# Kernel optimization log

Measured on AMD Instinct MI355X. Metric: run time of the kernel, lower is better.

Reference implementation:

```python
import jax, jax.numpy as jnp
import numpy as np

N = 100_000      # nodes
E = 20_000       # hyperedges
NNZ = 1_600_000  # pins (node, hyperedge) pairs
D_IN, D_HID, D_OUT = 128, 128, 64
EPS = 1e-5
NEG_SLOPE = 0.01


def _glorot(key, shape):
    fan_in, fan_out = shape
    lim = np.sqrt(6.0 / (fan_in + fan_out)).astype(np.float32)
    return jax.random.uniform(key, shape, jnp.float32, -lim, lim)


def setup_inputs() -> dict:
    key = jax.random.key(0)
    k = jax.random.split(key, 5)
    x = jax.random.normal(k[0], (N, D_IN), jnp.float32)
    node_idx = jax.random.randint(k[1], (NNZ,), 0, N)
    edge_idx = jax.random.randint(k[2], (NNZ,), 0, E)
    hyperedge_index = jnp.stack([node_idx, edge_idx]).astype(jnp.int64)
    return {
        "x": x,
        "hyperedge_index": hyperedge_index,
        "W1": _glorot(k[3], (D_IN, D_HID)),
        "b1": jnp.zeros((D_HID,), jnp.float32),
        "gamma": jnp.ones((D_HID,), jnp.float32),
        "beta": jnp.zeros((D_HID,), jnp.float32),
        "W3": _glorot(k[4], (D_HID, D_OUT)),
        "b3": jnp.zeros((D_OUT,), jnp.float32),
    }


def hypergraph_conv(x, node_idx, edge_idx, W, b):
    """PyG HypergraphConv (no attention, unit hyperedge weights):
    out = D^-1 H B H^T (x W) + b."""
    x = x @ W  # [N, F]
    ones = jnp.ones(node_idx.shape[0], x.dtype)
    Bdeg = jax.ops.segment_sum(ones, edge_idx, num_segments=E)  # hyperedge degree
    Ddeg = jax.ops.segment_sum(ones, node_idx, num_segments=N)  # node degree
    Binv = jnp.where(Bdeg > 0, 1.0 / Bdeg, 0.0)
    Dinv = jnp.where(Ddeg > 0, 1.0 / Ddeg, 0.0)
    # node -> hyperedge aggregation, scaled by B
    m = jax.ops.segment_sum(x[node_idx], edge_idx, num_segments=E) * Binv[:, None]
    # hyperedge -> node aggregation, scaled by D
    out = jax.ops.segment_sum(m[edge_idx], node_idx, num_segments=N) * Dinv[:, None]
    return out + b


def layer_norm(h, gamma, beta):
    mu = jnp.mean(h, axis=-1, keepdims=True)
    var = jnp.mean(jnp.square(h - mu), axis=-1, keepdims=True)
    return (h - mu) * jax.lax.rsqrt(var + EPS) * gamma + beta


def reference(x, hyperedge_index, W1, b1, gamma, beta, W3, b3):
    node_idx = hyperedge_index[0]
    edge_idx = hyperedge_index[1]
    h = hypergraph_conv(x, node_idx, edge_idx, W1, b1)
    h = layer_norm(h, gamma, beta)
    h = jax.nn.leaky_relu(h, NEG_SLOPE)
    # dropout is identity in eval mode
    z = hypergraph_conv(h, node_idx, edge_idx, W3, b3)
    return z
```

## Files before the change

### kernel.cpp

```cpp
#include <hip/hip_runtime.h>
#include <hip/hip_bf16.h>

#define NNODES 100000
#define NEDGES 20000
#define NPINS  1600000

#define EB_SHIFT 6
#define NB_SHIFT 7
#define NB_E ((NEDGES + 63) / 64)
#define NB_N ((NNODES + 127) / 128)
#define NB_TOT (NB_E + NB_N)
#define ECAP 6144
#define NCAP 2560
#define REG_TOTAL (NB_E * ECAP + NB_N * NCAP)

typedef __attribute__((ext_vector_type(8))) short short8;
typedef __attribute__((ext_vector_type(4))) float f32x4;
typedef unsigned int uint;


static __device__ inline float bf_lo(uint u) { return __uint_as_float(u << 16); }
static __device__ inline float bf_hi(uint u) { return __uint_as_float(u & 0xffff0000u); }

static __device__ inline uint pack_bf2(float a, float b) {
    union { __hip_bfloat16 h; unsigned short u; } ua, ub;
    ua.h = __float2bfloat16(a);
    ub.h = __float2bfloat16(b);
    return ((uint)ub.u << 16) | (uint)ua.u;
}


__global__ void __launch_bounds__(1024) bin_scatter(const int* __restrict__ he,
                                                    int* __restrict__ ccnt,
                                                    uint* __restrict__ pairs) {
    __shared__ int hcnt[NB_TOT];
    __shared__ int hbase[NB_TOT];
    int tid = threadIdx.x;
    int base = blockIdx.x * 8192;
    for (int j = tid; j < NB_TOT; j += 1024) hcnt[j] = 0;
    __syncthreads();
#pragma unroll
    for (int k = 0; k < 8; k++) {
        int i = base + k * 1024 + tid;
        if (i < NPINS) {
            int n = he[i];
            int e = he[NPINS + i];
            atomicAdd(&hcnt[e >> EB_SHIFT], 1);
            atomicAdd(&hcnt[NB_E + (n >> NB_SHIFT)], 1);
        }
    }
    __syncthreads();
    for (int j = tid; j < NB_TOT; j += 1024)
        hbase[j] = hcnt[j] ? atomicAdd(&ccnt[j], hcnt[j]) : 0;
    __syncthreads();
#pragma unroll
    for (int k = 0; k < 8; k++) {
        int i = base + k * 1024 + tid;
        if (i < NPINS) {
            int n = he[i];
            int e = he[NPINS + i];
            int be = e >> EB_SHIFT;
            int pe = atomicAdd(&hbase[be], 1);
            if (pe < ECAP)
                pairs[be * ECAP + pe] = ((uint)(e & 63) << 20) | (uint)n;
            int bn = n >> NB_SHIFT;
            int pn = atomicAdd(&hbase[NB_E + bn], 1);
            if (pn < NCAP)
                pairs[NB_E * ECAP + bn * NCAP + pn] = ((uint)(n & 127) << 20) | (uint)e;
        }
    }
}


template <int COLS, bool BF16IN>
static __device__ __forceinline__ void gemm_body(const void* __restrict__ Xv,
                                                 const float* __restrict__ W,
                                                 unsigned short* __restrict__ Yb,
                                                 long rowbase, char* lds) {
    char* Xl = lds;
    char* Wt = lds + 128 * 256;
    int tid = threadIdx.x;

    if constexpr (!BF16IN) {
        const float4* X4 = reinterpret_cast<const float4*>(Xv);
#pragma unroll
        for (int i = 0; i < 16; i++) {
            int f = tid + i * 256;
            int r = f >> 5;
            int c4 = f & 31;
            long gr = rowbase + r;
            if (gr > NNODES - 1) gr = NNODES - 1;
            float4 v = X4[gr * 32 + c4];
            uint lo = pack_bf2(v.x, v.y);
            uint hi = pack_bf2(v.z, v.w);
            int byte = r * 256 + ((c4 * 8) ^ ((r & 7) << 4));
            *reinterpret_cast<uint2*>(Xl + byte) = make_uint2(lo, hi);
        }
    } else {
        const uint4* X4 = reinterpret_cast<const uint4*>(Xv);
#pragma unroll
        for (int i = 0; i < 8; i++) {
            int f = tid + i * 256;
            int r = f >> 4;
            int c = f & 15;
            long gr = rowbase + r;
            if (gr > NNODES - 1) gr = NNODES - 1;
            uint4 v = X4[gr * 16 + c];
            int byte = r * 256 + ((c * 16) ^ ((r & 7) << 4));
            *reinterpret_cast<uint4*>(Xl + byte) = v;
        }
    }
    for (int f = tid; f < 128 * COLS / 4; f += 256) {
        int k = f / (COLS / 4);
        int c4 = f % (COLS / 4);
        float4 v = reinterpret_cast<const float4*>(W)[f];
        float vv[4] = {v.x, v.y, v.z, v.w};
#pragma unroll
        for (int j = 0; j < 4; j++) {
            int c = c4 * 4 + j;
            union { __hip_bfloat16 h; short s; } u;
            u.h = __float2bfloat16(vv[j]);
            int byte = c * 256 + ((k * 2) ^ ((c & 7) << 4));
            *reinterpret_cast<short*>(Wt + byte) = u.s;
        }
    }
    __syncthreads();

    constexpr int NF = COLS / 16;
    int wave = tid >> 6;
    int lane = tid & 63;
    int lrow = lane & 15;
    int lq = lane >> 4;
    f32x4 acc[2][NF] = {};

#pragma unroll
    for (int ks = 0; ks < 4; ks++) {
        short8 a[2];
#pragma unroll
        for (int rt = 0; rt < 2; rt++) {
            int r = wave * 32 + rt * 16 + lrow;
            int byte = r * 256 + ((ks * 64 + lq * 16) ^ ((r & 7) << 4));
            a[rt] = *reinterpret_cast<const short8*>(Xl + byte);
        }
#pragma unroll
        for (int nf = 0; nf < NF; nf++) {
            int c = nf * 16 + lrow;
            int byte = c * 256 + ((ks * 64 + lq * 16) ^ ((c & 7) << 4));
            short8 b = *reinterpret_cast<const short8*>(Wt + byte);
            acc[0][nf] = __builtin_amdgcn_mfma_f32_16x16x32_bf16(a[0], b, acc[0][nf], 0, 0, 0);
            acc[1][nf] = __builtin_amdgcn_mfma_f32_16x16x32_bf16(a[1], b, acc[1][nf], 0, 0, 0);
        }
    }

#pragma unroll
    for (int rt = 0; rt < 2; rt++)
#pragma unroll
        for (int nf = 0; nf < NF; nf++)
#pragma unroll
            for (int r = 0; r < 4; r++) {
                long row = rowbase + wave * 32 + rt * 16 + lq * 4 + r;
                if (row < NNODES) {
                    union { __hip_bfloat16 h; unsigned short u; } u;
                    u.h = __float2bfloat16(acc[rt][nf][r]);
                    Yb[row * COLS + nf * 16 + lrow] = u.u;
                }
            }
}

__global__ void gemm1_kernel(const float* __restrict__ x, const float* __restrict__ W,
                             unsigned short* __restrict__ Yb) {
    __shared__ __align__(16) char lds[128 * 256 + 128 * 256];
    gemm_body<128, false>(x, W, Yb, (long)blockIdx.x * 128, lds);
}

__global__ void gemm2_kernel(const void* __restrict__ Xv, const float* __restrict__ W,
                             unsigned short* __restrict__ Yb) {
    __shared__ __align__(16) char lds[128 * 256 + 64 * 256];
    gemm_body<64, true>(Xv, W, Yb, (long)blockIdx.x * 128, lds);
}


template <int KPB, int CAP>
static __device__ __forceinline__ void place_body(const uint* __restrict__ pairs, int regbase,
                                                  const int* __restrict__ ccnt, int cbase,
                                                  int kfine_base, int nkeys,
                                                  int* __restrict__ off, int* __restrict__ cnt,
                                                  int* __restrict__ pins, int b,
                                                  int* fh, int* fo, int* fcur) {
    constexpr int NIT = CAP / 256;
    int tid = threadIdx.x;
    int rb = regbase + b * CAP;
    int count = ccnt[cbase + b];
    if (count > CAP) count = CAP;
    int keyfirst = b * KPB;
    uint pr[NIT];
    for (int k = tid; k < KPB; k += 256) { fh[k] = 0; fcur[k] = 0; }
#pragma unroll
    for (int i = 0; i < NIT; i++) {
        int idx = tid + i * 256;
        if (idx < count) pr[i] = pairs[rb + idx];
    }
    __syncthreads();
#pragma unroll
    for (int i = 0; i < NIT; i++) {
        int idx = tid + i * 256;
        if (idx < count) atomicAdd(&fh[pr[i] >> 20], 1);
    }
    __syncthreads();
    if (tid == 0) {
        int run = rb;
        for (int k = 0; k < KPB; k++) { fo[k] = run; run += fh[k]; }
    }
    __syncthreads();
    for (int k = tid; k < KPB; k += 256) {
        int key = keyfirst + k;
        if (key < nkeys) { off[kfine_base + key] = fo[k]; cnt[kfine_base + key] = fh[k]; }
    }
#pragma unroll
    for (int i = 0; i < NIT; i++) {
        int idx = tid + i * 256;
        if (idx < count) {
            uint p = pr[i];
            int kl = (int)(p >> 20);
            int pos = atomicAdd(&fcur[kl], 1);
            pins[fo[kl] + pos] = (int)(p & 0xFFFFFu);
        }
    }
}

__global__ void k2_place(const uint* __restrict__ pairs, const int* __restrict__ ccnt,
                         int* __restrict__ off, int* __restrict__ cnt,
                         int* __restrict__ pins) {
    __shared__ int fh[128], fo[128], fcur[128];
    int b = blockIdx.x;
    if (b < NB_E)
        place_body<64, ECAP>(pairs, 0, ccnt, 0, 0, NEDGES, off, cnt, pins, b, fh, fo, fcur);
    else
        place_body<128, NCAP>(pairs, NB_E * ECAP, ccnt, NB_E, NEDGES, NNODES, off, cnt, pins,
                              b - NB_E, fh, fo, fcur);
}


#define ACC_U4(u) do { \
    a0 += bf_lo((u).x); a1 += bf_hi((u).x); a2 += bf_lo((u).y); a3 += bf_hi((u).y); \
    a4 += bf_lo((u).z); a5 += bf_hi((u).z); a6 += bf_lo((u).w); a7 += bf_hi((u).w); } while (0)

#define RED2(x, o1, o2) do { x += __shfl_xor(x, o1); x += __shfl_xor(x, o2); } while (0)
#define REDQ(o1, o2) do { RED2(a0,o1,o2); RED2(a1,o1,o2); RED2(a2,o1,o2); RED2(a3,o1,o2); \
                          RED2(a4,o1,o2); RED2(a5,o1,o2); RED2(a6,o1,o2); RED2(a7,o1,o2); } while (0)

__global__ void edge_agg_128(const uint4* __restrict__ feat4, const int* __restrict__ pins,
                             const int* __restrict__ off, const int* __restrict__ cnt,
                             uint4* __restrict__ outp) {
    int s = blockIdx.x * 4 + (threadIdx.x >> 6);
    if (s >= NEDGES) return;
    int lane = threadIdx.x & 63;
    int q = lane >> 4, fp = lane & 15;
    int start = off[s], c = cnt[s];
    float a0 = 0.f, a1 = 0.f, a2 = 0.f, a3 = 0.f, a4 = 0.f, a5 = 0.f, a6 = 0.f, a7 = 0.f;
    for (int cb = 0; cb < c; cb += 64) {
        int rem = c - cb;
        int lim = rem < 64 ? rem : 64;
        int pk = 0;
        if (lane < lim) pk = pins[start + cb + lane];
        int i = 0;
        for (; i + 16 <= lim; i += 16) {
            int pa = __shfl(pk, i + q);
            int pb = __shfl(pk, i + 4 + q);
            int pc = __shfl(pk, i + 8 + q);
            int pd = __shfl(pk, i + 12 + q);
            uint4 ua = feat4[(uint)pa * 16 + fp];
            uint4 ub = feat4[(uint)pb * 16 + fp];
            uint4 uc = feat4[(uint)pc * 16 + fp];
            uint4 ud = feat4[(uint)pd * 16 + fp];
            ACC_U4(ua); ACC_U4(ub); ACC_U4(uc); ACC_U4(ud);
        }
        for (; i + 4 <= lim; i += 4) {
            int p = __shfl(pk, i + q);
            uint4 u = feat4[(uint)p * 16 + fp];
            ACC_U4(u);
        }
        if (i < lim) {
            int idx = i + q;
            int p = __shfl(pk, idx < lim ? idx : i);
            if (idx < lim) {
                uint4 u = feat4[(uint)p * 16 + fp];
                ACC_U4(u);
            }
        }
    }
    REDQ(16, 32);
    if (q == 0) {
        float inv = (c > 0) ? (1.f / (float)c) : 0.f;
        outp[(uint)s * 16 + fp] = make_uint4(pack_bf2(a0 * inv, a1 * inv),
                                             pack_bf2(a2 * inv, a3 * inv),
                                             pack_bf2(a4 * inv, a5 * inv),
                                             pack_bf2(a6 * inv, a7 * inv));
    }
}

__global__ void node_agg_ln(const uint4* __restrict__ m4, const int* __restrict__ pins,
                            const int* __restrict__ off, const int* __restrict__ cnt,
                            const float* __restrict__ b1, const float* __restrict__ gamma,
                            const float* __restrict__ beta, uint4* __restrict__ hout) {
    int s = blockIdx.x * 4 + (threadIdx.x >> 6);
    if (s >= NNODES) return;
    int lane = threadIdx.x & 63;
    int q = lane >> 4, fp = lane & 15;
    int start = off[s], c = cnt[s];
    float a0 = 0.f, a1 = 0.f, a2 = 0.f, a3 = 0.f, a4 = 0.f, a5 = 0.f, a6 = 0.f, a7 = 0.f;
    for (int cb = 0; cb < c; cb += 64) {
        int rem = c - cb;
        int lim = rem < 64 ? rem : 64;
        int pk = 0;
        if (lane < lim) pk = pins[start + cb + lane];
        int i = 0;
        for (; i + 16 <= lim; i += 16) {
            int pa = __shfl(pk, i + q);
            int pb = __shfl(pk, i + 4 + q);
            int pc = __shfl(pk, i + 8 + q);
            int pd = __shfl(pk, i + 12 + q);
            uint4 ua = m4[(uint)pa * 16 + fp];
            uint4 ub = m4[(uint)pb * 16 + fp];
            uint4 uc = m4[(uint)pc * 16 + fp];
            uint4 ud = m4[(uint)pd * 16 + fp];
            ACC_U4(ua); ACC_U4(ub); ACC_U4(uc); ACC_U4(ud);
        }
        for (; i + 4 <= lim; i += 4) {
            int p = __shfl(pk, i + q);
            uint4 u = m4[(uint)p * 16 + fp];
            ACC_U4(u);
        }
        if (i < lim) {
            int idx = i + q;
            int p = __shfl(pk, idx < lim ? idx : i);
            if (idx < lim) {
                uint4 u = m4[(uint)p * 16 + fp];
                ACC_U4(u);
            }
        }
    }
    REDQ(16, 32);
    float dinv = (c > 0) ? (1.f / (float)c) : 0.f;
    float4 bb0 = reinterpret_cast<const float4*>(b1)[fp * 2];
    float4 bb1 = reinterpret_cast<const float4*>(b1)[fp * 2 + 1];
    float v0 = a0 * dinv + bb0.x;
    float v1 = a1 * dinv + bb0.y;
    float v2 = a2 * dinv + bb0.z;
    float v3 = a3 * dinv + bb0.w;
    float v4 = a4 * dinv + bb1.x;
    float v5 = a5 * dinv + bb1.y;
    float v6 = a6 * dinv + bb1.z;
    float v7 = a7 * dinv + bb1.w;
    float sum = ((v0 + v1) + (v2 + v3)) + ((v4 + v5) + (v6 + v7));
    float sq = ((v0 * v0 + v1 * v1) + (v2 * v2 + v3 * v3)) +
               ((v4 * v4 + v5 * v5) + (v6 * v6 + v7 * v7));
#pragma unroll
    for (int o = 1; o < 16; o <<= 1) {
        sum += __shfl_xor(sum, o);
        sq  += __shfl_xor(sq, o);
    }
    float mu = sum * (1.f / 128.f);
    float var = sq * (1.f / 128.f) - mu * mu;
    float rstd = rsqrtf(var + 1e-5f);
    if (q == 0) {
        float4 g0  = reinterpret_cast<const float4*>(gamma)[fp * 2];
        float4 g1  = reinterpret_cast<const float4*>(gamma)[fp * 2 + 1];
        float4 be0 = reinterpret_cast<const float4*>(beta)[fp * 2];
        float4 be1 = reinterpret_cast<const float4*>(beta)[fp * 2 + 1];
        float h0 = (v0 - mu) * rstd * g0.x + be0.x;
        float h1 = (v1 - mu) * rstd * g0.y + be0.y;
        float h2 = (v2 - mu) * rstd * g0.z + be0.z;
        float h3 = (v3 - mu) * rstd * g0.w + be0.w;
        float h4 = (v4 - mu) * rstd * g1.x + be1.x;
        float h5 = (v5 - mu) * rstd * g1.y + be1.y;
        float h6 = (v6 - mu) * rstd * g1.z + be1.z;
        float h7 = (v7 - mu) * rstd * g1.w + be1.w;
        h0 = (h0 > 0.f) ? h0 : 0.01f * h0;
        h1 = (h1 > 0.f) ? h1 : 0.01f * h1;
        h2 = (h2 > 0.f) ? h2 : 0.01f * h2;
        h3 = (h3 > 0.f) ? h3 : 0.01f * h3;
        h4 = (h4 > 0.f) ? h4 : 0.01f * h4;
        h5 = (h5 > 0.f) ? h5 : 0.01f * h5;
        h6 = (h6 > 0.f) ? h6 : 0.01f * h6;
        h7 = (h7 > 0.f) ? h7 : 0.01f * h7;
        hout[(uint)s * 16 + fp] = make_uint4(pack_bf2(h0, h1), pack_bf2(h2, h3),
                                             pack_bf2(h4, h5), pack_bf2(h6, h7));
    }
}

#define REDE(o1, o2, o3) do { \
    a0 += __shfl_xor(a0, o1); a0 += __shfl_xor(a0, o2); a0 += __shfl_xor(a0, o3); \
    a1 += __shfl_xor(a1, o1); a1 += __shfl_xor(a1, o2); a1 += __shfl_xor(a1, o3); \
    a2 += __shfl_xor(a2, o1); a2 += __shfl_xor(a2, o2); a2 += __shfl_xor(a2, o3); \
    a3 += __shfl_xor(a3, o1); a3 += __shfl_xor(a3, o2); a3 += __shfl_xor(a3, o3); \
    a4 += __shfl_xor(a4, o1); a4 += __shfl_xor(a4, o2); a4 += __shfl_xor(a4, o3); \
    a5 += __shfl_xor(a5, o1); a5 += __shfl_xor(a5, o2); a5 += __shfl_xor(a5, o3); \
    a6 += __shfl_xor(a6, o1); a6 += __shfl_xor(a6, o2); a6 += __shfl_xor(a6, o3); \
    a7 += __shfl_xor(a7, o1); a7 += __shfl_xor(a7, o2); a7 += __shfl_xor(a7, o3); } while (0)

__global__ void edge_agg_64(const uint4* __restrict__ feat4, const int* __restrict__ pins,
                            const int* __restrict__ off, const int* __restrict__ cnt,
                            uint4* __restrict__ outp) {
    int s = blockIdx.x * 4 + (threadIdx.x >> 6);
    if (s >= NEDGES) return;
    int lane = threadIdx.x & 63;
    int e = lane >> 3, fp = lane & 7;
    int start = off[s], c = cnt[s];
    float a0 = 0.f, a1 = 0.f, a2 = 0.f, a3 = 0.f, a4 = 0.f, a5 = 0.f, a6 = 0.f, a7 = 0.f;
    for (int cb = 0; cb < c; cb += 64) {
        int rem = c - cb;
        int lim = rem < 64 ? rem : 64;
        int pk = 0;
        if (lane < lim) pk = pins[start + cb + lane];
        int i = 0;
        for (; i + 32 <= lim; i += 32) {
            int pa = __shfl(pk, i + e);
            int pb = __shfl(pk, i + 8 + e);
            int pc = __shfl(pk, i + 16 + e);
            int pd = __shfl(pk, i + 24 + e);
            uint4 ua = feat4[(uint)pa * 8 + fp];
            uint4 ub = feat4[(uint)pb * 8 + fp];
            uint4 uc = feat4[(uint)pc * 8 + fp];
            uint4 ud = feat4[(uint)pd * 8 + fp];
            ACC_U4(ua); ACC_U4(ub); ACC_U4(uc); ACC_U4(ud);
        }
        for (; i + 8 <= lim; i += 8) {
            int p = __shfl(pk, i + e);
            uint4 u = feat4[(uint)p * 8 + fp];
            ACC_U4(u);
        }
        if (i < lim) {
            int idx = i + e;
            int p = __shfl(pk, idx < lim ? idx : i);
            if (idx < lim) {
                uint4 u = feat4[(uint)p * 8 + fp];
                ACC_U4(u);
            }
        }
    }
    REDE(8, 16, 32);
    if (e == 0) {
        float inv = (c > 0) ? (1.f / (float)c) : 0.f;
        outp[(uint)s * 8 + fp] = make_uint4(pack_bf2(a0 * inv, a1 * inv),
                                            pack_bf2(a2 * inv, a3 * inv),
                                            pack_bf2(a4 * inv, a5 * inv),
                                            pack_bf2(a6 * inv, a7 * inv));
    }
}

__global__ void node_agg_out(const uint4* __restrict__ m4, const int* __restrict__ pins,
                             const int* __restrict__ off, const int* __restrict__ cnt,
                             const float* __restrict__ b3, float4* __restrict__ out4) {
    int s = blockIdx.x * 4 + (threadIdx.x >> 6);
    if (s >= NNODES) return;
    int lane = threadIdx.x & 63;
    int e = lane >> 3, fp = lane & 7;
    int start = off[s], c = cnt[s];
    float a0 = 0.f, a1 = 0.f, a2 = 0.f, a3 = 0.f, a4 = 0.f, a5 = 0.f, a6 = 0.f, a7 = 0.f;
    for (int cb = 0; cb < c; cb += 64) {
        int rem = c - cb;
        int lim = rem < 64 ? rem : 64;
        int pk = 0;
        if (lane < lim) pk = pins[start + cb + lane];
        int i = 0;
        for (; i + 32 <= lim; i += 32) {
            int pa = __shfl(pk, i + e);
            int pb = __shfl(pk, i + 8 + e);
            int pc = __shfl(pk, i + 16 + e);
            int pd = __shfl(pk, i + 24 + e);
            uint4 ua = m4[(uint)pa * 8 + fp];
            uint4 ub = m4[(uint)pb * 8 + fp];
            uint4 uc = m4[(uint)pc * 8 + fp];
            uint4 ud = m4[(uint)pd * 8 + fp];
            ACC_U4(ua); ACC_U4(ub); ACC_U4(uc); ACC_U4(ud);
        }
        for (; i + 8 <= lim; i += 8) {
            int p = __shfl(pk, i + e);
            uint4 u = m4[(uint)p * 8 + fp];
            ACC_U4(u);
        }
        if (i < lim) {
            int idx = i + e;
            int p = __shfl(pk, idx < lim ? idx : i);
            if (idx < lim) {
                uint4 u = m4[(uint)p * 8 + fp];
                ACC_U4(u);
            }
        }
    }
    REDE(8, 16, 32);
    if (e == 0) {
        float inv = (c > 0) ? (1.f / (float)c) : 0.f;
        float4 bb0 = reinterpret_cast<const float4*>(b3)[fp * 2];
        float4 bb1 = reinterpret_cast<const float4*>(b3)[fp * 2 + 1];
        out4[(uint)s * 16 + fp * 2] = make_float4(a0 * inv + bb0.x, a1 * inv + bb0.y,
                                                  a2 * inv + bb0.z, a3 * inv + bb0.w);
        out4[(uint)s * 16 + fp * 2 + 1] = make_float4(a4 * inv + bb1.x, a5 * inv + bb1.y,
                                                      a6 * inv + bb1.z, a7 * inv + bb1.w);
    }
}


extern "C" void kernel_launch(void* const* d_in, const int* in_sizes, int n_in,
                              void* d_out, int out_size, void* d_ws, size_t ws_size,
                              hipStream_t stream) {
    const float* x     = (const float*)d_in[0];
    const int*   he    = (const int*)d_in[1];
    const float* W1    = (const float*)d_in[2];
    const float* b1    = (const float*)d_in[3];
    const float* gamma = (const float*)d_in[4];
    const float* beta  = (const float*)d_in[5];
    const float* W3    = (const float*)d_in[6];
    const float* b3    = (const float*)d_in[7];
    float* out = (float*)d_out;

    char* ws = (char*)d_ws;
    uint* xWb = (uint*)ws;
    uint* mb  = (uint*)(ws + 25600000);
    uint* hb  = (uint*)(ws + 30720000);
    char* ip  = ws + 56320000;
    int* off  = (int*)ip;
    int* cnt  = off + (NEDGES + NNODES);
    int* ccnt = cnt + (NEDGES + NNODES);
    int* pins = ccnt + NB_TOT + 64;
    uint* pairs = (uint*)(ws + 73400000);

    hipMemsetAsync(ccnt, 0, sizeof(int) * NB_TOT, stream);
    bin_scatter<<<(NPINS + 8191) / 8192, 1024, 0, stream>>>(he, ccnt, pairs);
    k2_place<<<NB_TOT, 256, 0, stream>>>(pairs, ccnt, off, cnt, pins);

    gemm1_kernel<<<(NNODES + 127) / 128, 256, 0, stream>>>(x, W1, (unsigned short*)xWb);
    edge_agg_128<<<(NEDGES + 3) / 4, 256, 0, stream>>>((const uint4*)xWb, pins, off, cnt,
                                                       (uint4*)mb);
    node_agg_ln<<<(NNODES + 3) / 4, 256, 0, stream>>>((const uint4*)mb, pins, off + NEDGES,
                                                      cnt + NEDGES, b1, gamma, beta,
                                                      (uint4*)hb);
    gemm2_kernel<<<(NNODES + 127) / 128, 256, 0, stream>>>(hb, W3, (unsigned short*)xWb);
    edge_agg_64<<<(NEDGES + 3) / 4, 256, 0, stream>>>((const uint4*)xWb, pins, off, cnt,
                                                      (uint4*)mb);
    node_agg_out<<<(NNODES + 3) / 4, 256, 0, stream>>>((const uint4*)mb, pins, off + NEDGES,
                                                       cnt + NEDGES, b3, (float4*)out);
}
```

Before: 277.2 us.

## Replace block-local histogram binning with 4-way sharded global atomic counters

```diff
diff --git a/kernel.cpp b/kernel.cpp
--- a/kernel.cpp
+++ b/kernel.cpp
@@ -12,6 +12,8 @@
 #define NB_TOT (NB_E + NB_N)
 #define ECAP 6144
 #define NCAP 2560
+#define ECAPS (ECAP / 4)
+#define NCAPS (NCAP / 4)
 #define REG_TOTAL (NB_E * ECAP + NB_N * NCAP)
 
 typedef __attribute__((ext_vector_type(8))) short short8;
@@ -30,43 +32,25 @@
 }
 
 
-__global__ void __launch_bounds__(1024) bin_scatter(const int* __restrict__ he,
-                                                    int* __restrict__ ccnt,
-                                                    uint* __restrict__ pairs) {
-    __shared__ int hcnt[NB_TOT];
-    __shared__ int hbase[NB_TOT];
-    int tid = threadIdx.x;
-    int base = blockIdx.x * 8192;
-    for (int j = tid; j < NB_TOT; j += 1024) hcnt[j] = 0;
-    __syncthreads();
-#pragma unroll
-    for (int k = 0; k < 8; k++) {
-        int i = base + k * 1024 + tid;
-        if (i < NPINS) {
-            int n = he[i];
-            int e = he[NPINS + i];
-            atomicAdd(&hcnt[e >> EB_SHIFT], 1);
-            atomicAdd(&hcnt[NB_E + (n >> NB_SHIFT)], 1);
-        }
-    }
-    __syncthreads();
-    for (int j = tid; j < NB_TOT; j += 1024)
-        hbase[j] = hcnt[j] ? atomicAdd(&ccnt[j], hcnt[j]) : 0;
-    __syncthreads();
-#pragma unroll
-    for (int k = 0; k < 8; k++) {
-        int i = base + k * 1024 + tid;
+__global__ void bin_scatter(const int* __restrict__ he, int* __restrict__ ccnt4,
+                            uint* __restrict__ pairs) {
+    int sh = blockIdx.x & 3;
+    int base = blockIdx.x * 1024;
+#pragma unroll
+    for (int k = 0; k < 4; k++) {
+        int i = base + k * 256 + threadIdx.x;
         if (i < NPINS) {
             int n = he[i];
             int e = he[NPINS + i];
             int be = e >> EB_SHIFT;
-            int pe = atomicAdd(&hbase[be], 1);
-            if (pe < ECAP)
-                pairs[be * ECAP + pe] = ((uint)(e & 63) << 20) | (uint)n;
+            int pe = atomicAdd(&ccnt4[be * 4 + sh], 1);
+            if (pe < ECAPS)
+                pairs[be * ECAP + sh * ECAPS + pe] = ((uint)(e & 63) << 20) | (uint)n;
             int bn = n >> NB_SHIFT;
-            int pn = atomicAdd(&hbase[NB_E + bn], 1);
-            if (pn < NCAP)
-                pairs[NB_E * ECAP + bn * NCAP + pn] = ((uint)(n & 127) << 20) | (uint)e;
+            int pn = atomicAdd(&ccnt4[(NB_E + bn) * 4 + sh], 1);
+            if (pn < NCAPS)
+                pairs[NB_E * ECAP + bn * NCAP + sh * NCAPS + pn] =
+                    ((uint)(n & 127) << 20) | (uint)e;
         }
     }
 }
@@ -182,30 +166,35 @@
 
 template <int KPB, int CAP>
 static __device__ __forceinline__ void place_body(const uint* __restrict__ pairs, int regbase,
-                                                  const int* __restrict__ ccnt, int cbase,
+                                                  const int* __restrict__ ccnt4, int cbase,
                                                   int kfine_base, int nkeys,
                                                   int* __restrict__ off, int* __restrict__ cnt,
                                                   int* __restrict__ pins, int b,
-                                                  int* fh, int* fo, int* fcur) {
+                                                  int* fh, int* fo, int* fcur, int* cs) {
+    constexpr int CAPS = CAP / 4;
     constexpr int NIT = CAP / 256;
     int tid = threadIdx.x;
     int rb = regbase + b * CAP;
-    int count = ccnt[cbase + b];
-    if (count > CAP) count = CAP;
     int keyfirst = b * KPB;
+    if (tid < 4) {
+        int c = ccnt4[(cbase + b) * 4 + tid];
+        cs[tid] = c > CAPS ? CAPS : c;
+    }
+    for (int k = tid; k < KPB; k += 256) { fh[k] = 0; fcur[k] = 0; }
+    __syncthreads();
     uint pr[NIT];
-    for (int k = tid; k < KPB; k += 256) { fh[k] = 0; fcur[k] = 0; }
+    bool vld[NIT];
 #pragma unroll
     for (int i = 0; i < NIT; i++) {
         int idx = tid + i * 256;
-        if (idx < count) pr[i] = pairs[rb + idx];
-    }
-    __syncthreads();
-#pragma unroll
-    for (int i = 0; i < NIT; i++) {
-        int idx = tid + i * 256;
-        if (idx < count) atomicAdd(&fh[pr[i] >> 20], 1);
-    }
+        int s = idx / CAPS;
+        int local = idx - s * CAPS;
+        vld[i] = local < cs[s];
+        if (vld[i]) pr[i] = pairs[rb + idx];
+    }
+#pragma unroll
+    for (int i = 0; i < NIT; i++)
+        if (vld[i]) atomicAdd(&fh[pr[i] >> 20], 1);
     __syncthreads();
     if (tid == 0) {
         int run = rb;
@@ -217,27 +206,26 @@
         if (key < nkeys) { off[kfine_base + key] = fo[k]; cnt[kfine_base + key] = fh[k]; }
     }
 #pragma unroll
-    for (int i = 0; i < NIT; i++) {
-        int idx = tid + i * 256;
-        if (idx < count) {
+    for (int i = 0; i < NIT; i++)
+        if (vld[i]) {
             uint p = pr[i];
             int kl = (int)(p >> 20);
             int pos = atomicAdd(&fcur[kl], 1);
             pins[fo[kl] + pos] = (int)(p & 0xFFFFFu);
         }
-    }
-}
-
-__global__ void k2_place(const uint* __restrict__ pairs, const int* __restrict__ ccnt,
+}
+
+__global__ void k2_place(const uint* __restrict__ pairs, const int* __restrict__ ccnt4,
                          int* __restrict__ off, int* __restrict__ cnt,
                          int* __restrict__ pins) {
-    __shared__ int fh[128], fo[128], fcur[128];
+    __shared__ int fh[128], fo[128], fcur[128], cs[4];
     int b = blockIdx.x;
     if (b < NB_E)
-        place_body<64, ECAP>(pairs, 0, ccnt, 0, 0, NEDGES, off, cnt, pins, b, fh, fo, fcur);
+        place_body<64, ECAP>(pairs, 0, ccnt4, 0, 0, NEDGES, off, cnt, pins, b,
+                             fh, fo, fcur, cs);
     else
-        place_body<128, NCAP>(pairs, NB_E * ECAP, ccnt, NB_E, NEDGES, NNODES, off, cnt, pins,
-                              b - NB_E, fh, fo, fcur);
+        place_body<128, NCAP>(pairs, NB_E * ECAP, ccnt4, NB_E, NEDGES, NNODES, off, cnt, pins,
+                              b - NB_E, fh, fo, fcur, cs);
 }
 
 
@@ -520,15 +508,15 @@
     uint* mb  = (uint*)(ws + 25600000);
     uint* hb  = (uint*)(ws + 30720000);
     char* ip  = ws + 56320000;
-    int* off  = (int*)ip;
-    int* cnt  = off + (NEDGES + NNODES);
-    int* ccnt = cnt + (NEDGES + NNODES);
-    int* pins = ccnt + NB_TOT + 64;
+    int* off   = (int*)ip;
+    int* cnt   = off + (NEDGES + NNODES);
+    int* ccnt4 = cnt + (NEDGES + NNODES);
+    int* pins  = ccnt4 + NB_TOT * 4 + 64;
     uint* pairs = (uint*)(ws + 73400000);
 
-    hipMemsetAsync(ccnt, 0, sizeof(int) * NB_TOT, stream);
-    bin_scatter<<<(NPINS + 8191) / 8192, 1024, 0, stream>>>(he, ccnt, pairs);
-    k2_place<<<NB_TOT, 256, 0, stream>>>(pairs, ccnt, off, cnt, pins);
+    hipMemsetAsync(ccnt4, 0, sizeof(int) * NB_TOT * 4, stream);
+    bin_scatter<<<(NPINS + 1023) / 1024, 256, 0, stream>>>(he, ccnt4, pairs);
+    k2_place<<<NB_TOT, 256, 0, stream>>>(pairs, ccnt4, off, cnt, pins);
 
     gemm1_kernel<<<(NNODES + 127) / 128, 256, 0, stream>>>(x, W1, (unsigned short*)xWb);
     edge_agg_128<<<(NEDGES + 3) / 4, 256, 0, stream>>>((const uint4*)xWb, pins, off, cnt,
```

Result: slower. 566.2 us (+104.3%).
